# Performance work log

Hardware: AMD Instinct MI355X
Metric: run time of the kernel (lower is better)

The kernel has to match this reference:

```python
import jax, jax.numpy as jnp
import numpy as np

NUM_HEADS = 16

def setup_inputs() -> dict:
    key = jax.random.key(0)
    ks = jax.random.split(key, 7)
    B, Nq, Nkv, D = 4, 1024, 4096, 1024
    q = jax.random.normal(ks[0], (B, Nq, D), dtype=jnp.float32)
    kv = jax.random.normal(ks[1], (B, Nkv, D), dtype=jnp.float32)
    # True = padded key; keep position 0 unmasked so no row is fully masked
    mask = jax.random.randint(ks[2], (B, Nkv), 0, 2) > 0
    mask = mask.at[:, 0].set(False)
    s = D ** -0.5
    Wq = jax.random.normal(ks[3], (D, D), dtype=jnp.float32) * s
    Wkv = jax.random.normal(ks[4], (D, 2 * D), dtype=jnp.float32) * s
    Wproj = jax.random.normal(ks[5], (D, D), dtype=jnp.float32) * s
    bproj = jnp.zeros((D,), dtype=jnp.float32)
    return {"q": q, "kv": kv, "key_padding_mask": mask,
            "Wq": Wq, "Wkv": Wkv, "Wproj": Wproj, "bproj": bproj}

def reference(q, kv, key_padding_mask, Wq, Wkv, Wproj, bproj):
    B, Nq, D = q.shape
    Nkv = kv.shape[1]
    H = NUM_HEADS
    hd = D // H
    scale = hd ** -0.5
    # projections (qkv_bias=False)
    qp = (q @ Wq).reshape(B, Nq, H, hd).transpose(0, 2, 1, 3) * scale  # (B,H,Nq,hd)
    kvp = kv @ Wkv  # (B,Nkv,2D); first D -> k, last D -> v
    k = kvp[..., :D].reshape(B, Nkv, H, hd).transpose(0, 2, 1, 3)  # (B,H,Nkv,hd)
    v = kvp[..., D:].reshape(B, Nkv, H, hd).transpose(0, 2, 1, 3)
    attn = jnp.einsum('bhqd,bhkd->bhqk', qp, k)  # (B,H,Nq,Nkv)
    neg_inf = jnp.finfo(attn.dtype).min
    attn = jnp.where(key_padding_mask[:, None, None, :], neg_inf, attn)
    attn = jax.nn.softmax(attn, axis=-1)
    x = jnp.einsum('bhqk,bhkd->bhqd', attn, v)  # (B,H,Nq,hd)
    x = x.transpose(0, 2, 1, 3).reshape(B, Nq, D)
    return x @ Wproj + bproj
```

## Files before the change

kernel.cpp:

```cpp
#include <hip/hip_runtime.h>
#include <hip/hip_bf16.h>
#include <math.h>

#define BB 4
#define NQ 1024
#define NKV 4096
#define DMODEL 1024
#define NH 16
#define HD 64

typedef __attribute__((ext_vector_type(8))) short short8;
typedef __attribute__((ext_vector_type(4))) float floatx4;

__device__ __forceinline__ unsigned short f2bf(float f) {
    __hip_bfloat16 b = __float2bfloat16(f);
    return *reinterpret_cast<unsigned short*>(&b);
}

__device__ __forceinline__ unsigned int pack2bf_rhu(float a, float b) {
    unsigned ua = __builtin_bit_cast(unsigned, a) + 0x8000u;
    unsigned ub = __builtin_bit_cast(unsigned, b) + 0x8000u;
    return (ua >> 16) | (ub & 0xffff0000u);
}

__device__ __forceinline__ void gl_lds16(void* lds, const void* g) {
    __builtin_amdgcn_global_load_lds(
        (const __attribute__((address_space(1))) unsigned int*)g,
        (__attribute__((address_space(3))) unsigned int*)lds, 16, 0, 0);
}

__global__ __launch_bounds__(1024) void maskprep2(const int* __restrict__ mask,
                                                  float* __restrict__ maskadd) {
    __shared__ int s;
    if (threadIdx.x == 0) s = 0;
    __syncthreads();
    int local = 0;
    for (int i = threadIdx.x; i < 4096; i += 1024)
        if (((const unsigned*)mask)[i] > 1u) local = 1;
    if (local) atomicOr(&s, 1);
    __syncthreads();
    const bool bytes = (s != 0);
    for (int i = threadIdx.x; i < BB * NKV; i += 1024) {
        bool m = bytes ? (((const unsigned char*)mask)[i] != 0) : (mask[i] != 0);
        maskadd[i] = m ? -1e30f : 0.0f;
    }
}

__global__ __launch_bounds__(256) void cast_bf16(const float* __restrict__ src,
                                                 unsigned short* __restrict__ dst,
                                                 int n) {
    int i = (blockIdx.x * 256 + threadIdx.x) * 8;
    if (i >= n) return;
    float4 a = *(const float4*)&src[i];
    float4 b = *(const float4*)&src[i + 4];
    short8 v;
    v[0] = (short)f2bf(a.x); v[1] = (short)f2bf(a.y);
    v[2] = (short)f2bf(a.z); v[3] = (short)f2bf(a.w);
    v[4] = (short)f2bf(b.x); v[5] = (short)f2bf(b.y);
    v[6] = (short)f2bf(b.z); v[7] = (short)f2bf(b.w);
    *(short8*)&dst[i] = v;
}

__global__ __launch_bounds__(256) void transpose_cast3(
    const float* __restrict__ Wq, const float* __restrict__ Wkv,
    const float* __restrict__ Wproj,
    unsigned short* __restrict__ WqT, unsigned short* __restrict__ WkvT,
    unsigned short* __restrict__ WprojT)
{
    const float* src; unsigned short* dst; int N;
    if (blockIdx.z == 0)      { src = Wq;    dst = WqT;    N = DMODEL; }
    else if (blockIdx.z == 1) { src = Wkv;   dst = WkvT;   N = 2 * DMODEL; }
    else                      { src = Wproj; dst = WprojT; N = DMODEL; }
    if ((int)blockIdx.x * 64 >= N) return;
    const int K = DMODEL;
    __shared__ unsigned short t[64][72];
    int r0 = blockIdx.y * 64, c0 = blockIdx.x * 64;
    int tid = threadIdx.x;
#pragma unroll
    for (int i = 0; i < 4; i++) {
        int r = i * 16 + (tid >> 4), c = (tid & 15) * 4;
        float4 v = *(const float4*)&src[(size_t)(r0 + r) * N + c0 + c];
        t[c + 0][r] = f2bf(v.x); t[c + 1][r] = f2bf(v.y);
        t[c + 2][r] = f2bf(v.z); t[c + 3][r] = f2bf(v.w);
    }
    __syncthreads();
#pragma unroll
    for (int i = 0; i < 2; i++) {
        int rr = i * 32 + (tid >> 3), cc = (tid & 7) * 8;
        *(uint4*)&dst[(size_t)(c0 + rr) * K + r0 + cc] = *(uint4*)&t[rr][cc];
    }
}

template <int EPI>
__global__ __launch_bounds__(256) void gemm_mfma(
    const unsigned short* __restrict__ A,
    const unsigned short* __restrict__ Bt,
    const float* __restrict__ bias,
    unsigned short* __restrict__ o16,
    unsigned short* __restrict__ oT,
    float* __restrict__ o32,
    int M, int N, int K, float alpha, int m_out_base)
{
    extern __shared__ char smem[];
    unsigned short* As = (unsigned short*)smem;
    unsigned short* Bs = (unsigned short*)(smem + 8192);
    const int tid = threadIdx.x;
    const int wave = tid >> 6, lane = tid & 63;
    const int quad = lane >> 4, l16 = lane & 15;
    const int wm = wave >> 1, wn = wave & 1;
    const int m0 = blockIdx.y * 128, n0 = blockIdx.x * 128;

    const int c0 = wave * 64 + lane, c1 = c0 + 256;
    const int r0s = c0 >> 2, cc0 = (c0 & 3) ^ ((r0s >> 2) & 3);
    const int r1s = c1 >> 2, cc1 = (c1 & 3) ^ ((r1s >> 2) & 3);
    const unsigned short* ag0 = A + (size_t)(m0 + r0s) * K + cc0 * 8;
    const unsigned short* ag1 = A + (size_t)(m0 + r1s) * K + cc1 * 8;
    const unsigned short* bg0 = Bt + (size_t)(n0 + r0s) * K + cc0 * 8;
    const unsigned short* bg1 = Bt + (size_t)(n0 + r1s) * K + cc1 * 8;
    char* AldsW0 = (char*)As + (wave * 64) * 16;
    char* AldsW1 = (char*)As + (256 + wave * 64) * 16;
    char* BldsW0 = (char*)Bs + (wave * 64) * 16;
    char* BldsW1 = (char*)Bs + (256 + wave * 64) * 16;

    int achk[4], bchk[4];
#pragma unroll
    for (int i = 0; i < 4; i++) {
        int ra = wm * 64 + i * 16 + l16;
        achk[i] = ra * 4 + (quad ^ ((ra >> 2) & 3));
        int rb = wn * 64 + i * 16 + l16;
        bchk[i] = rb * 4 + (quad ^ ((rb >> 2) & 3));
    }

    floatx4 acc[4][4];
#pragma unroll
    for (int i = 0; i < 4; i++)
#pragma unroll
        for (int j = 0; j < 4; j++) acc[i][j] = (floatx4)0.0f;

    for (int kt = 0; kt < K; kt += 32) {
        __syncthreads();
        gl_lds16(AldsW0, ag0 + kt);
        gl_lds16(AldsW1, ag1 + kt);
        gl_lds16(BldsW0, bg0 + kt);
        gl_lds16(BldsW1, bg1 + kt);
        __syncthreads();
        short8 af[4], bfr[4];
#pragma unroll
        for (int i = 0; i < 4; i++) af[i] = *(const short8*)&As[achk[i] * 8];
#pragma unroll
        for (int j = 0; j < 4; j++) bfr[j] = *(const short8*)&Bs[bchk[j] * 8];
#pragma unroll
        for (int i = 0; i < 4; i++)
#pragma unroll
            for (int j = 0; j < 4; j++)
                acc[i][j] = __builtin_amdgcn_mfma_f32_16x16x32_bf16(
                    af[i], bfr[j], acc[i][j], 0, 0, 0);
    }

    const int rowbase = m0 + wm * 64;
    const int colbase = n0 + wn * 64;
    if (EPI == 0) {
#pragma unroll
        for (int i = 0; i < 4; i++)
#pragma unroll
            for (int r = 0; r < 4; r++) {
                size_t row = (size_t)(rowbase + i * 16 + quad * 4 + r);
#pragma unroll
                for (int j = 0; j < 4; j++)
                    o16[row * N + colbase + j * 16 + l16] =
                        f2bf(acc[i][j][r] * alpha);
            }
    } else if (EPI == 2) {
        float bv[4];
#pragma unroll
        for (int j = 0; j < 4; j++) bv[j] = bias[colbase + j * 16 + l16];
#pragma unroll
        for (int i = 0; i < 4; i++)
#pragma unroll
            for (int r = 0; r < 4; r++) {
                size_t row = (size_t)(rowbase + i * 16 + quad * 4 + r);
#pragma unroll
                for (int j = 0; j < 4; j++)
                    o32[row * N + colbase + j * 16 + l16] = acc[i][j][r] + bv[j];
            }
    } else {
        if (n0 < DMODEL) {
#pragma unroll
            for (int i = 0; i < 4; i++)
#pragma unroll
                for (int r = 0; r < 4; r++) {
                    int gm = m_out_base + rowbase + i * 16 + quad * 4 + r;
                    int b = gm >> 12, key = gm & (NKV - 1);
                    size_t row = (size_t)(b * NKV + key);
#pragma unroll
                    for (int j = 0; j < 4; j++)
                        o16[row * DMODEL + colbase + j * 16 + l16] =
                            f2bf(acc[i][j][r]);
                }
        } else {
            __syncthreads();
            unsigned short (*scr)[72] =
                (unsigned short(*)[72])(smem + wave * 64 * 72 * 2);
#pragma unroll
            for (int i = 0; i < 4; i++)
#pragma unroll
                for (int j = 0; j < 4; j++)
#pragma unroll
                    for (int r = 0; r < 4; r++)
                        scr[j * 16 + l16][i * 16 + quad * 4 + r] =
                            f2bf(acc[i][j][r]);
            __syncthreads();
            int gmb = m_out_base + rowbase;
            int b = gmb >> 12, key0 = gmb & (NKV - 1);
            int d0 = colbase - DMODEL;
#pragma unroll
            for (int p = 0; p < 8; p++) {
                int rr = p * 8 + (lane >> 3), ch = lane & 7;
                *(uint4*)&oT[((size_t)(b * DMODEL + d0 + rr)) * NKV + key0 + ch * 8] =
                    *(uint4*)&scr[rr][ch * 8];
            }
        }
    }
}

__global__ __launch_bounds__(256, 3) void attn_mfma4(
    const unsigned short* __restrict__ Qb,
    const unsigned short* __restrict__ Kb,
    const unsigned short* __restrict__ VTb,
    const float* __restrict__ maskadd,
    unsigned short* __restrict__ x)
{
    const int lid = blockIdx.y * gridDim.x + blockIdx.x;
    const int xcd = lid & 7, slot = lid >> 3;
    const int bh = xcd * 8 + (slot & 7);
    const int b = bh >> 4, h = bh & 15;
    const int m0 = (slot >> 3) * 64;
    const int tid = threadIdx.x;
    const int wave = tid >> 6, lane = tid & 63;
    const int quad = lane >> 4, l16 = lane & 15;

    __shared__ __align__(16) unsigned short qp_s[64][72];
    __shared__ __align__(16) unsigned short k_s[2][64][72];
    __shared__ __align__(16) unsigned short vT_s[2][80][72];

    const int kr = tid >> 2, kc = (tid & 3) * 16;

    for (int t = tid; t < 2 * 16 * 72; t += 256) {
        int bufi = t / (16 * 72), rem = t % (16 * 72);
        vT_s[bufi][64 + rem / 72][rem % 72] = 0x3F80;
    }
    {
        const unsigned short* src =
            Qb + ((size_t)(b * NQ + m0 + kr)) * DMODEL + h * HD + kc;
        *(uint4*)&qp_s[kr][kc]     = *(const uint4*)src;
        *(uint4*)&qp_s[kr][kc + 8] = *(const uint4*)(src + 8);
    }

    const float* madd_row = maskadd + b * NKV;
    const unsigned short* Kbase = Kb + ((size_t)b * NKV) * DMODEL + h * HD;
    const unsigned short* Vbase = VTb + ((size_t)(b * DMODEL + h * HD)) * NKV;

    {
        const unsigned short* ks = Kbase + (size_t)kr * DMODEL + kc;
        uint4 a0 = *(const uint4*)ks, a1 = *(const uint4*)(ks + 8);
        const unsigned short* vs = Vbase + (size_t)kr * NKV + kc;
        uint4 b0 = *(const uint4*)vs, b1 = *(const uint4*)(vs + 8);
        *(uint4*)&k_s[0][kr][kc]      = a0;
        *(uint4*)&k_s[0][kr][kc + 8]  = a1;
        *(uint4*)&vT_s[0][kr][kc]     = b0;
        *(uint4*)&vT_s[0][kr][kc + 8] = b1;
    }
    __syncthreads();

    short8 bq0 = *(const short8*)&qp_s[wave * 16 + l16][quad * 8];
    short8 bq1 = *(const short8*)&qp_s[wave * 16 + l16][32 + quad * 8];

    floatx4 o[4], ol;
#pragma unroll
    for (int f = 0; f < 4; f++) o[f] = (floatx4)0.0f;
    ol = (floatx4)0.0f;
    unsigned short* prow = &qp_s[wave * 16 + l16][0];

    for (int i = 0; i < NKV / 64; i++) {
        const int buf = i & 1;
        uint4 pk0, pk1, pv0, pv1;
        const bool pf = (i < NKV / 64 - 1);
        if (pf) {
            int nn = (i + 1) * 64;
            const unsigned short* ks = Kbase + (size_t)(nn + kr) * DMODEL + kc;
            pk0 = *(const uint4*)ks; pk1 = *(const uint4*)(ks + 8);
            const unsigned short* vs = Vbase + (size_t)kr * NKV + nn + kc;
            pv0 = *(const uint4*)vs; pv1 = *(const uint4*)(vs + 8);
        }
        if (i) __syncthreads();

        floatx4 st[4];
#pragma unroll
        for (int f = 0; f < 4; f++) {
            short8 ak0 = *(const short8*)&k_s[buf][f * 16 + l16][quad * 8];
            short8 ak1 = *(const short8*)&k_s[buf][f * 16 + l16][32 + quad * 8];
            floatx4 t = (floatx4)0.0f;
            t = __builtin_amdgcn_mfma_f32_16x16x32_bf16(ak0, bq0, t, 0, 0, 0);
            t = __builtin_amdgcn_mfma_f32_16x16x32_bf16(ak1, bq1, t, 0, 0, 0);
            st[f] = t;
        }

        int n0 = i * 64;
#pragma unroll
        for (int f = 0; f < 4; f++) {
            float4 mv = *(const float4*)&madd_row[n0 + f * 16 + quad * 4];
            float p0 = __builtin_amdgcn_exp2f(st[f][0] + mv.x);
            float p1 = __builtin_amdgcn_exp2f(st[f][1] + mv.y);
            float p2 = __builtin_amdgcn_exp2f(st[f][2] + mv.z);
            float p3 = __builtin_amdgcn_exp2f(st[f][3] + mv.w);
            uint2 pw;
            pw.x = pack2bf_rhu(p0, p1);
            pw.y = pack2bf_rhu(p2, p3);
            *(uint2*)&prow[f * 16 + quad * 4] = pw;
        }

        asm volatile("s_waitcnt lgkmcnt(0)" ::: "memory");
        short8 ap0 = *(const short8*)&qp_s[wave * 16 + l16][quad * 8];
        short8 ap1 = *(const short8*)&qp_s[wave * 16 + l16][32 + quad * 8];
#pragma unroll
        for (int f = 0; f < 4; f++) {
            short8 bv0 = *(const short8*)&vT_s[buf][f * 16 + l16][quad * 8];
            short8 bv1 = *(const short8*)&vT_s[buf][f * 16 + l16][32 + quad * 8];
            o[f] = __builtin_amdgcn_mfma_f32_16x16x32_bf16(ap0, bv0, o[f], 0, 0, 0);
            o[f] = __builtin_amdgcn_mfma_f32_16x16x32_bf16(ap1, bv1, o[f], 0, 0, 0);
        }
        {
            short8 bv0 = *(const short8*)&vT_s[buf][64 + l16][quad * 8];
            short8 bv1 = *(const short8*)&vT_s[buf][64 + l16][32 + quad * 8];
            ol = __builtin_amdgcn_mfma_f32_16x16x32_bf16(ap0, bv0, ol, 0, 0, 0);
            ol = __builtin_amdgcn_mfma_f32_16x16x32_bf16(ap1, bv1, ol, 0, 0, 0);
        }

        if (pf) {
            *(uint4*)&k_s[buf ^ 1][kr][kc]      = pk0;
            *(uint4*)&k_s[buf ^ 1][kr][kc + 8]  = pk1;
            *(uint4*)&vT_s[buf ^ 1][kr][kc]     = pv0;
            *(uint4*)&vT_s[buf ^ 1][kr][kc + 8] = pv1;
        }
    }

#pragma unroll
    for (int r = 0; r < 4; r++) {
        float inv = 1.0f / ol[r];
        size_t row = (size_t)(b * NQ + m0 + wave * 16 + quad * 4 + r);
#pragma unroll
        for (int f = 0; f < 4; f++) {
            unsigned u = __builtin_bit_cast(unsigned, o[f][r] * inv) + 0x8000u;
            x[row * DMODEL + h * HD + f * 16 + l16] = (unsigned short)(u >> 16);
        }
    }
}

extern "C" void kernel_launch(void* const* d_in, const int* in_sizes, int n_in,
                              void* d_out, int out_size, void* d_ws, size_t ws_size,
                              hipStream_t stream) {
    const float* q     = (const float*)d_in[0];
    const float* kv    = (const float*)d_in[1];
    const int*   mask  = (const int*)d_in[2];
    const float* Wq    = (const float*)d_in[3];
    const float* Wkv   = (const float*)d_in[4];
    const float* Wproj = (const float*)d_in[5];
    const float* bproj = (const float*)d_in[6];
    float* out = (float*)d_out;

    char* ws = (char*)d_ws;
    size_t o = 0;
    o += 256;
    float* maskadd   = (float*)(ws + o); o += 65536;
    unsigned short* Qb     = (unsigned short*)(ws + o); o += (size_t)BB * NQ * DMODEL * 2;
    unsigned short* Kb     = (unsigned short*)(ws + o); o += (size_t)BB * NKV * DMODEL * 2;
    unsigned short* VTb    = (unsigned short*)(ws + o); o += (size_t)BB * NKV * DMODEL * 2;
    unsigned short* WprojT = (unsigned short*)(ws + o); o += (size_t)DMODEL * DMODEL * 2;
    unsigned short* qbf    = (unsigned short*)(ws + o);
    unsigned short* xb     = qbf;
    o += (size_t)BB * NQ * DMODEL * 2;
    unsigned short* WqT    = (unsigned short*)(ws + o); o += (size_t)DMODEL * DMODEL * 2;
    unsigned short* WkvT   = (unsigned short*)(ws + o); o += (size_t)DMODEL * 2 * DMODEL * 2;
    unsigned short* kvh = (unsigned short*)d_out;

    hipLaunchKernelGGL(maskprep2, dim3(1), dim3(1024), 0, stream, mask, maskadd);
    hipLaunchKernelGGL(transpose_cast3, dim3(32, DMODEL / 64, 3), dim3(256), 0, stream,
                       Wq, Wkv, Wproj, WqT, WkvT, WprojT);

    hipLaunchKernelGGL(cast_bf16, dim3(BB * NQ * DMODEL / 2048), dim3(256), 0, stream,
                       q, qbf, BB * NQ * DMODEL);
    hipLaunchKernelGGL((gemm_mfma<0>), dim3(DMODEL / 128, BB * NQ / 128), dim3(256), 16384, stream,
                       qbf, WqT, (const float*)nullptr, Qb, (unsigned short*)nullptr,
                       (float*)nullptr, BB * NQ, DMODEL, DMODEL, 0.125f * 1.44269504f, 0);

    const int HALF_ROWS = BB * NKV / 2;
    for (int half = 0; half < 2; half++) {
        const float* src = kv + (size_t)half * HALF_ROWS * DMODEL;
        hipLaunchKernelGGL(cast_bf16, dim3(HALF_ROWS * DMODEL / 2048), dim3(256), 0, stream,
                           src, kvh, HALF_ROWS * DMODEL);
        hipLaunchKernelGGL((gemm_mfma<1>), dim3(2 * DMODEL / 128, HALF_ROWS / 128), dim3(256), 36864, stream,
                           kvh, WkvT, (const float*)nullptr, Kb, VTb,
                           (float*)nullptr, HALF_ROWS, 2 * DMODEL, DMODEL, 1.0f, half * HALF_ROWS);
    }

    hipLaunchKernelGGL(attn_mfma4, dim3(NQ / 64, BB * NH), dim3(256), 0, stream,
                       Qb, Kb, VTb, maskadd, xb);

    hipLaunchKernelGGL((gemm_mfma<2>), dim3(DMODEL / 128, BB * NQ / 128), dim3(256), 16384, stream,
                       xb, WprojT, bproj, (unsigned short*)nullptr, (unsigned short*)nullptr,
                       out, BB * NQ, DMODEL, DMODEL, 1.0f, 0);
}
```

Baseline: 456.8 us.

## Enlarge attention query tile to 128 rows with 512-thread blocks

The attention kernel now processes 128 query rows per block using 8 waves instead of 64 rows with 4 waves. Each K/V tile loaded into shared memory is reused by twice as many queries, halving K/V global traffic per query. The load mapping is redistributed so each thread fetches one uint4 each of K and V per step. The grid halves, which may reduce parallelism and raises register and LDS pressure per block; the block-to-XCD mapping formula is kept unchanged.

```diff
diff --git a/kernel.cpp b/kernel.cpp
--- a/kernel.cpp
+++ b/kernel.cpp
@@ -223,7 +223,7 @@
     }
 }
 
-__global__ __launch_bounds__(256, 3) void attn_mfma4(
+__global__ __launch_bounds__(512, 4) void attn_mfma5(
     const unsigned short* __restrict__ Qb,
     const unsigned short* __restrict__ Kb,
     const unsigned short* __restrict__ VTb,
@@ -234,41 +234,40 @@
     const int xcd = lid & 7, slot = lid >> 3;
     const int bh = xcd * 8 + (slot & 7);
     const int b = bh >> 4, h = bh & 15;
-    const int m0 = (slot >> 3) * 64;
+    const int m0 = (slot >> 3) * 128;
     const int tid = threadIdx.x;
     const int wave = tid >> 6, lane = tid & 63;
     const int quad = lane >> 4, l16 = lane & 15;
 
-    __shared__ __align__(16) unsigned short qp_s[64][72];
+    __shared__ __align__(16) unsigned short qp_s[128][72];
     __shared__ __align__(16) unsigned short k_s[2][64][72];
     __shared__ __align__(16) unsigned short vT_s[2][80][72];
 
-    const int kr = tid >> 2, kc = (tid & 3) * 16;
-
-    for (int t = tid; t < 2 * 16 * 72; t += 256) {
+    for (int t = tid; t < 2 * 16 * 72; t += 512) {
         int bufi = t / (16 * 72), rem = t % (16 * 72);
         vT_s[bufi][64 + rem / 72][rem % 72] = 0x3F80;
     }
     {
+        const int qr = tid >> 2, qc = (tid & 3) * 16;
         const unsigned short* src =
-            Qb + ((size_t)(b * NQ + m0 + kr)) * DMODEL + h * HD + kc;
-        *(uint4*)&qp_s[kr][kc]     = *(const uint4*)src;
-        *(uint4*)&qp_s[kr][kc + 8] = *(const uint4*)(src + 8);
+            Qb + ((size_t)(b * NQ + m0 + qr)) * DMODEL + h * HD + qc;
+        *(uint4*)&qp_s[qr][qc]     = *(const uint4*)src;
+        *(uint4*)&qp_s[qr][qc + 8] = *(const uint4*)(src + 8);
     }
 
     const float* madd_row = maskadd + b * NKV;
     const unsigned short* Kbase = Kb + ((size_t)b * NKV) * DMODEL + h * HD;
     const unsigned short* Vbase = VTb + ((size_t)(b * DMODEL + h * HD)) * NKV;
 
+    const int kr = tid >> 3, kc = (tid & 7) * 8;
+
     {
         const unsigned short* ks = Kbase + (size_t)kr * DMODEL + kc;
-        uint4 a0 = *(const uint4*)ks, a1 = *(const uint4*)(ks + 8);
+        uint4 a0 = *(const uint4*)ks;
         const unsigned short* vs = Vbase + (size_t)kr * NKV + kc;
-        uint4 b0 = *(const uint4*)vs, b1 = *(const uint4*)(vs + 8);
-        *(uint4*)&k_s[0][kr][kc]      = a0;
-        *(uint4*)&k_s[0][kr][kc + 8]  = a1;
-        *(uint4*)&vT_s[0][kr][kc]     = b0;
-        *(uint4*)&vT_s[0][kr][kc + 8] = b1;
+        uint4 b0 = *(const uint4*)vs;
+        *(uint4*)&k_s[0][kr][kc]  = a0;
+        *(uint4*)&vT_s[0][kr][kc] = b0;
     }
     __syncthreads();
 
@@ -283,14 +282,12 @@
 
     for (int i = 0; i < NKV / 64; i++) {
         const int buf = i & 1;
-        uint4 pk0, pk1, pv0, pv1;
+        uint4 pk, pv;
         const bool pf = (i < NKV / 64 - 1);
         if (pf) {
             int nn = (i + 1) * 64;
-            const unsigned short* ks = Kbase + (size_t)(nn + kr) * DMODEL + kc;
-            pk0 = *(const uint4*)ks; pk1 = *(const uint4*)(ks + 8);
-            const unsigned short* vs = Vbase + (size_t)kr * NKV + nn + kc;
-            pv0 = *(const uint4*)vs; pv1 = *(const uint4*)(vs + 8);
+            pk = *(const uint4*)(Kbase + (size_t)(nn + kr) * DMODEL + kc);
+            pv = *(const uint4*)(Vbase + (size_t)kr * NKV + nn + kc);
         }
         if (i) __syncthreads();
 
@@ -337,10 +334,8 @@
         }
 
         if (pf) {
-            *(uint4*)&k_s[buf ^ 1][kr][kc]      = pk0;
-            *(uint4*)&k_s[buf ^ 1][kr][kc + 8]  = pk1;
-            *(uint4*)&vT_s[buf ^ 1][kr][kc]     = pv0;
-            *(uint4*)&vT_s[buf ^ 1][kr][kc + 8] = pv1;
+            *(uint4*)&k_s[buf ^ 1][kr][kc]  = pk;
+            *(uint4*)&vT_s[buf ^ 1][kr][kc] = pv;
         }
     }
 
@@ -403,7 +398,7 @@
                            (float*)nullptr, HALF_ROWS, 2 * DMODEL, DMODEL, 1.0f, half * HALF_ROWS);
     }
 
-    hipLaunchKernelGGL(attn_mfma4, dim3(NQ / 64, BB * NH), dim3(256), 0, stream,
+    hipLaunchKernelGGL(attn_mfma5, dim3(NQ / 128, BB * NH), dim3(512), 0, stream,
                        Qb, Kb, VTb, maskadd, xb);
 
     hipLaunchKernelGGL((gemm_mfma<2>), dim3(DMODEL / 128, BB * NQ / 128), dim3(256), 16384, stream,
```

New measurement: 423.4 us. 1.08x faster.

## Double query tile per attention block and compute row sums without ones-column MFMA

Applied to the files above, without the earlier changes.

The attention kernel now processes 128 query rows per block: each wave handles two 16-row subtiles and reuses the same K and V fragments from shared memory for both. This halves how often K/V tiles are loaded per query row. The row-sum trick (an extra ones-padded V block fed through MFMA) is replaced by summing the rounded bf16 probabilities in registers and reducing them with lane shuffles at the end. In exchange, registers per thread rise and the occupancy bound drops from 3 to 2 blocks, and the grid is half as large.

```diff
diff --git a/kernel.cpp b/kernel.cpp
--- a/kernel.cpp
+++ b/kernel.cpp
@@ -223,7 +223,7 @@
     }
 }
 
-__global__ __launch_bounds__(256, 3) void attn_mfma4(
+__global__ __launch_bounds__(256, 2) void attn_mfma6(
     const unsigned short* __restrict__ Qb,
     const unsigned short* __restrict__ Kb,
     const unsigned short* __restrict__ VTb,
@@ -234,31 +234,30 @@
     const int xcd = lid & 7, slot = lid >> 3;
     const int bh = xcd * 8 + (slot & 7);
     const int b = bh >> 4, h = bh & 15;
-    const int m0 = (slot >> 3) * 64;
+    const int m0 = (slot >> 3) * 128;
     const int tid = threadIdx.x;
     const int wave = tid >> 6, lane = tid & 63;
     const int quad = lane >> 4, l16 = lane & 15;
 
-    __shared__ __align__(16) unsigned short qp_s[64][72];
+    __shared__ __align__(16) unsigned short qp_s[128][72];
     __shared__ __align__(16) unsigned short k_s[2][64][72];
-    __shared__ __align__(16) unsigned short vT_s[2][80][72];
-
-    const int kr = tid >> 2, kc = (tid & 3) * 16;
-
-    for (int t = tid; t < 2 * 16 * 72; t += 256) {
-        int bufi = t / (16 * 72), rem = t % (16 * 72);
-        vT_s[bufi][64 + rem / 72][rem % 72] = 0x3F80;
-    }
+    __shared__ __align__(16) unsigned short vT_s[2][64][72];
+
     {
+        const int qr = tid >> 1, qc = (tid & 1) * 32;
         const unsigned short* src =
-            Qb + ((size_t)(b * NQ + m0 + kr)) * DMODEL + h * HD + kc;
-        *(uint4*)&qp_s[kr][kc]     = *(const uint4*)src;
-        *(uint4*)&qp_s[kr][kc + 8] = *(const uint4*)(src + 8);
+            Qb + ((size_t)(b * NQ + m0 + qr)) * DMODEL + h * HD + qc;
+        *(uint4*)&qp_s[qr][qc]      = *(const uint4*)src;
+        *(uint4*)&qp_s[qr][qc + 8]  = *(const uint4*)(src + 8);
+        *(uint4*)&qp_s[qr][qc + 16] = *(const uint4*)(src + 16);
+        *(uint4*)&qp_s[qr][qc + 24] = *(const uint4*)(src + 24);
     }
 
     const float* madd_row = maskadd + b * NKV;
     const unsigned short* Kbase = Kb + ((size_t)b * NKV) * DMODEL + h * HD;
     const unsigned short* Vbase = VTb + ((size_t)(b * DMODEL + h * HD)) * NKV;
+
+    const int kr = tid >> 2, kc = (tid & 3) * 16;
 
     {
         const unsigned short* ks = Kbase + (size_t)kr * DMODEL + kc;
@@ -272,14 +271,21 @@
     }
     __syncthreads();
 
-    short8 bq0 = *(const short8*)&qp_s[wave * 16 + l16][quad * 8];
-    short8 bq1 = *(const short8*)&qp_s[wave * 16 + l16][32 + quad * 8];
-
-    floatx4 o[4], ol;
-#pragma unroll
-    for (int f = 0; f < 4; f++) o[f] = (floatx4)0.0f;
-    ol = (floatx4)0.0f;
-    unsigned short* prow = &qp_s[wave * 16 + l16][0];
+    short8 bq[2][2];
+#pragma unroll
+    for (int s = 0; s < 2; s++) {
+        bq[s][0] = *(const short8*)&qp_s[wave * 32 + s * 16 + l16][quad * 8];
+        bq[s][1] = *(const short8*)&qp_s[wave * 32 + s * 16 + l16][32 + quad * 8];
+    }
+
+    floatx4 o[2][4];
+#pragma unroll
+    for (int s = 0; s < 2; s++)
+#pragma unroll
+        for (int f = 0; f < 4; f++) o[s][f] = (floatx4)0.0f;
+    float lsum[2] = {0.0f, 0.0f};
+    unsigned short* prow0 = &qp_s[wave * 32 + l16][0];
+    unsigned short* prow1 = &qp_s[wave * 32 + 16 + l16][0];
 
     for (int i = 0; i < NKV / 64; i++) {
         const int buf = i & 1;
@@ -294,46 +300,63 @@
         }
         if (i) __syncthreads();
 
-        floatx4 st[4];
+        short8 ak[4][2], bv[4][2];
 #pragma unroll
         for (int f = 0; f < 4; f++) {
-            short8 ak0 = *(const short8*)&k_s[buf][f * 16 + l16][quad * 8];
-            short8 ak1 = *(const short8*)&k_s[buf][f * 16 + l16][32 + quad * 8];
-            floatx4 t = (floatx4)0.0f;
-            t = __builtin_amdgcn_mfma_f32_16x16x32_bf16(ak0, bq0, t, 0, 0, 0);
-            t = __builtin_amdgcn_mfma_f32_16x16x32_bf16(ak1, bq1, t, 0, 0, 0);
-            st[f] = t;
-        }
-
-        int n0 = i * 64;
-#pragma unroll
-        for (int f = 0; f < 4; f++) {
-            float4 mv = *(const float4*)&madd_row[n0 + f * 16 + quad * 4];
-            float p0 = __builtin_amdgcn_exp2f(st[f][0] + mv.x);
-            float p1 = __builtin_amdgcn_exp2f(st[f][1] + mv.y);
-            float p2 = __builtin_amdgcn_exp2f(st[f][2] + mv.z);
-            float p3 = __builtin_amdgcn_exp2f(st[f][3] + mv.w);
-            uint2 pw;
-            pw.x = pack2bf_rhu(p0, p1);
-            pw.y = pack2bf_rhu(p2, p3);
-            *(uint2*)&prow[f * 16 + quad * 4] = pw;
+            ak[f][0] = *(const short8*)&k_s[buf][f * 16 + l16][quad * 8];
+            ak[f][1] = *(const short8*)&k_s[buf][f * 16 + l16][32 + quad * 8];
+            bv[f][0] = *(const short8*)&vT_s[buf][f * 16 + l16][quad * 8];
+            bv[f][1] = *(const short8*)&vT_s[buf][f * 16 + l16][32 + quad * 8];
+        }
+
+        const int n0 = i * 64;
+        float4 mv[4];
+#pragma unroll
+        for (int f = 0; f < 4; f++)
+            mv[f] = *(const float4*)&madd_row[n0 + f * 16 + quad * 4];
+
+#pragma unroll
+        for (int s = 0; s < 2; s++) {
+            floatx4 st[4];
+#pragma unroll
+            for (int f = 0; f < 4; f++) {
+                floatx4 t = (floatx4)0.0f;
+                t = __builtin_amdgcn_mfma_f32_16x16x32_bf16(ak[f][0], bq[s][0], t, 0, 0, 0);
+                t = __builtin_amdgcn_mfma_f32_16x16x32_bf16(ak[f][1], bq[s][1], t, 0, 0, 0);
+                st[f] = t;
+            }
+            unsigned short* prow = s ? prow1 : prow0;
+            float ls = 0.0f;
+#pragma unroll
+            for (int f = 0; f < 4; f++) {
+                float p0 = __builtin_amdgcn_exp2f(st[f][0] + mv[f].x);
+                float p1 = __builtin_amdgcn_exp2f(st[f][1] + mv[f].y);
+                float p2 = __builtin_amdgcn_exp2f(st[f][2] + mv[f].z);
+                float p3 = __builtin_amdgcn_exp2f(st[f][3] + mv[f].w);
+                uint2 pw;
+                pw.x = pack2bf_rhu(p0, p1);
+                pw.y = pack2bf_rhu(p2, p3);
+                *(uint2*)&prow[f * 16 + quad * 4] = pw;
+                float r0 = __builtin_bit_cast(float, pw.x << 16);
+                float r1 = __builtin_bit_cast(float, pw.x & 0xffff0000u);
+                float r2 = __builtin_bit_cast(float, pw.y << 16);
+                float r3 = __builtin_bit_cast(float, pw.y & 0xffff0000u);
+                ls += (r0 + r1) + (r2 + r3);
+            }
+            lsum[s] += ls;
         }
 
         asm volatile("s_waitcnt lgkmcnt(0)" ::: "memory");
-        short8 ap0 = *(const short8*)&qp_s[wave * 16 + l16][quad * 8];
-        short8 ap1 = *(const short8*)&qp_s[wave * 16 + l16][32 + quad * 8];
-#pragma unroll
-        for (int f = 0; f < 4; f++) {
-            short8 bv0 = *(const short8*)&vT_s[buf][f * 16 + l16][quad * 8];
-            short8 bv1 = *(const short8*)&vT_s[buf][f * 16 + l16][32 + quad * 8];
-            o[f] = __builtin_amdgcn_mfma_f32_16x16x32_bf16(ap0, bv0, o[f], 0, 0, 0);
-            o[f] = __builtin_amdgcn_mfma_f32_16x16x32_bf16(ap1, bv1, o[f], 0, 0, 0);
-        }
-        {
-            short8 bv0 = *(const short8*)&vT_s[buf][64 + l16][quad * 8];
-            short8 bv1 = *(const short8*)&vT_s[buf][64 + l16][32 + quad * 8];
-            ol = __builtin_amdgcn_mfma_f32_16x16x32_bf16(ap0, bv0, ol, 0, 0, 0);
-            ol = __builtin_amdgcn_mfma_f32_16x16x32_bf16(ap1, bv1, ol, 0, 0, 0);
+#pragma unroll
+        for (int s = 0; s < 2; s++) {
+            const unsigned short* pr = s ? prow1 : prow0;
+            short8 ap0 = *(const short8*)&pr[quad * 8];
+            short8 ap1 = *(const short8*)&pr[32 + quad * 8];
+#pragma unroll
+            for (int f = 0; f < 4; f++) {
+                o[s][f] = __builtin_amdgcn_mfma_f32_16x16x32_bf16(ap0, bv[f][0], o[s][f], 0, 0, 0);
+                o[s][f] = __builtin_amdgcn_mfma_f32_16x16x32_bf16(ap1, bv[f][1], o[s][f], 0, 0, 0);
+            }
         }
 
         if (pf) {
@@ -345,13 +368,21 @@
     }
 
 #pragma unroll
-    for (int r = 0; r < 4; r++) {
-        float inv = 1.0f / ol[r];
-        size_t row = (size_t)(b * NQ + m0 + wave * 16 + quad * 4 + r);
-#pragma unroll
-        for (int f = 0; f < 4; f++) {
-            unsigned u = __builtin_bit_cast(unsigned, o[f][r] * inv) + 0x8000u;
-            x[row * DMODEL + h * HD + f * 16 + l16] = (unsigned short)(u >> 16);
+    for (int s = 0; s < 2; s++) {
+        float t = lsum[s];
+        t += __shfl_xor(t, 16);
+        t += __shfl_xor(t, 32);
+        size_t rowb = (size_t)(b * NQ + m0 + wave * 32 + s * 16);
+#pragma unroll
+        for (int r = 0; r < 4; r++) {
+            float lr = __shfl(t, quad * 4 + r);
+            float inv = 1.0f / lr;
+            size_t row = rowb + quad * 4 + r;
+#pragma unroll
+            for (int f = 0; f < 4; f++) {
+                unsigned u = __builtin_bit_cast(unsigned, o[s][f][r] * inv) + 0x8000u;
+                x[row * DMODEL + h * HD + f * 16 + l16] = (unsigned short)(u >> 16);
+            }
         }
     }
 }
@@ -403,7 +434,7 @@
                            (float*)nullptr, HALF_ROWS, 2 * DMODEL, DMODEL, 1.0f, half * HALF_ROWS);
     }
 
-    hipLaunchKernelGGL(attn_mfma4, dim3(NQ / 64, BB * NH), dim3(256), 0, stream,
+    hipLaunchKernelGGL(attn_mfma6, dim3(NQ / 128, BB * NH), dim3(256), 0, stream,
                        Qb, Kb, VTb, maskadd, xb);
 
     hipLaunchKernelGGL((gemm_mfma<2>), dim3(DMODEL / 128, BB * NQ / 128), dim3(256), 16384, stream,
```

New measurement: 422.7 us. 1.08x faster.
